# Performance work log

Measured on AMD Instinct MI355X. Metric: run time of the kernel, lower is better.

The kernel has to match this reference:

```python
import jax, jax.numpy as jnp
import numpy as np

LEAKAGE = 0.9
RADIUS = 0.1
AVG_DEGREE = 6


def setup_inputs() -> dict:
    key = jax.random.key(0)
    k1, k2, k3, k4, k5 = jax.random.split(key, 5)
    B, T, I, N, O = 16, 2048, 32, 2048, 32
    input_sequence = jax.random.normal(k1, (B, T, I), dtype=jnp.float32)
    # sparse reservoir matrix, uniform(-1,1) with density avg_degree/N, scaled to spectral radius
    A = jax.random.uniform(k2, (N, N), minval=-1.0, maxval=1.0, dtype=jnp.float32)
    mask = jax.random.uniform(k3, (N, N)) < (AVG_DEGREE / N)
    A = jnp.where(mask, A, 0.0)
    # approximate spectral normalization (power-iteration-free surrogate scale)
    A = A * (RADIUS / jnp.max(jnp.abs(jnp.linalg.eigvals(A))).astype(jnp.float32))
    Win = (RADIUS) * (2.0 * jax.random.uniform(k4, (N, I), dtype=jnp.float32) - 1.0)
    Wout_w = jax.random.normal(k5, (O, N), dtype=jnp.float32) / np.sqrt(N)
    return {"input_sequence": input_sequence, "Win": Win, "A": A, "Wout_w": Wout_w, "washout_len": 64}


def reference(input_sequence, Win, A, Wout_w, washout_len):
    # input projection for all timesteps at once (noise_std = 0.0)
    inp = jnp.einsum('bti,ni->btn', input_sequence, Win)  # [B, T, N]
    B = input_sequence.shape[0]
    N = A.shape[0]
    h0 = jnp.zeros((B, N), dtype=input_sequence.dtype)
    At = A.T

    def step(h, u_t):
        # h: [B, N], u_t: [B, N]
        h_new = (1.0 - LEAKAGE) * h + LEAKAGE * jnp.tanh(h @ At + u_t)
        return h_new, h_new

    _, hs = jax.lax.scan(step, h0, jnp.swapaxes(inp, 0, 1))  # hs: [T, B, N]
    hs = jnp.swapaxes(hs, 0, 1)  # [B, T, N]
    h_list = hs[:, washout_len - 1:]  # keep steps i >= washout_len - 1
    return jnp.einsum('btn,on->bto', h_list, Wout_w)
```

## Files before the change

kernel.cpp:

```cpp
#include <hip/hip_runtime.h>
#include <stdint.h>

#define BB 16
#define TT 2048
#define NI 32
#define NN 2048
#define NO 32
#define WASH 64
#define TO (TT - WASH + 1)
#define W 24
#define WT 24
#define CH 16
#define HBST 2056
#define HBROW 4112
#define UROWB 4136
#define U2OFF 65792
#define LDS_BYTES (U2OFF + CH*UROWB)

typedef short bfvec __attribute__((ext_vector_type(8)));
typedef float f4_t  __attribute__((ext_vector_type(4)));

__device__ inline unsigned short f2bf(float f) {
  unsigned int u = __builtin_bit_cast(unsigned int, f);
  unsigned int r = u + 0x7fffu + ((u >> 16) & 1u);
  return (unsigned short)(r >> 16);
}
__device__ inline float bf2f(unsigned short s) {
  unsigned int u = ((unsigned int)s) << 16;
  return __builtin_bit_cast(float, u);
}
__device__ inline float tanh_fast(float x) {
  x = fminf(15.f, fmaxf(-15.f, x));
  float e = __expf(x + x);
  float r = __builtin_amdgcn_rcpf(e + 1.0f);
  return (e - 1.0f) * r;
}

__global__ void build_ell(const float* __restrict__ A, uint32_t* __restrict__ ell,
                          uint32_t* __restrict__ deg) {
  int gw = (int)((blockIdx.x * blockDim.x + threadIdx.x) >> 6);
  int lane = (int)(threadIdx.x & 63);
  if (gw >= NN) return;
  const float* row = A + (size_t)gw * NN;
  int base = 0;
  for (int c = 0; c < NN; c += 64) {
    float v = row[c + lane];
    bool nz = (v != 0.0f);
    unsigned long long mask = __ballot(nz);
    int pre = __popcll(mask & ((1ull << lane) - 1ull));
    if (nz) {
      int idx = base + pre;
      if (idx < W) {
        uint32_t packed = (((uint32_t)f2bf(v)) << 16) | (uint32_t)((c + lane) * 4);
        ell[(size_t)gw * W + idx] = packed;
      }
    }
    base += __popcll(mask);
  }
  int d = base < W ? base : W;
  if (lane == 0) deg[gw] = (uint32_t)d;
  for (int k = d + lane; k < W; k += 64) ell[(size_t)gw * W + k] = 0u;
}

__global__ void sortperm(const uint32_t* __restrict__ deg, uint32_t* __restrict__ perm,
                         uint32_t* __restrict__ invp) {
  __shared__ int dg[NN];
  int tid = (int)threadIdx.x;
  dg[tid] = (int)deg[tid];
  dg[tid + 1024] = (int)deg[tid + 1024];
  __syncthreads();
  for (int r = tid; r < NN; r += 1024) {
    int d = dg[r];
    int rank = 0;
    for (int j = 0; j < NN; ++j) {
      int dj = dg[j];
      rank += (dj < d) || (dj == d && j < r);
    }
    perm[rank] = (uint32_t)r;
    invp[r] = (uint32_t)rank;
  }
}

__global__ void pairsort(const uint32_t* __restrict__ deg, const uint32_t* __restrict__ perm,
                         uint32_t* __restrict__ pairrank, uint32_t* __restrict__ pp) {
  __shared__ int ps[1024];
  int p = (int)threadIdx.x;
  int d0 = (int)deg[perm[p]]; if (d0 > W) d0 = W;
  int d1 = (int)deg[perm[2047 - p]]; if (d1 > W) d1 = W;
  int s = d0 + d1; if (s > WT) s = WT;
  ps[p] = s;
  __syncthreads();
  int rank = 0;
  for (int j = 0; j < 1024; ++j) {
    int sj = ps[j];
    rank += (sj < s) || (sj == s && j < p);
  }
  pairrank[p] = (uint32_t)rank;
  pp[rank] = (uint32_t)p;
}

__device__ inline int rank2pos(int r, const uint32_t* pairrank) {
  return (r < 1024) ? (2 * (int)pairrank[r]) : (2 * (int)pairrank[2047 - r] + 1);
}

__global__ void build_pairs(const uint32_t* __restrict__ ell, const uint32_t* __restrict__ deg,
                            const uint32_t* __restrict__ perm, const uint32_t* __restrict__ invp,
                            const uint32_t* __restrict__ pairrank, const uint32_t* __restrict__ pp,
                            uint32_t* __restrict__ pa, uint32_t* __restrict__ pva,
                            uint32_t* __restrict__ pvb, uint32_t* __restrict__ wavecnt) {
  int blk = (int)blockIdx.x;
  int lane = (int)threadIdx.x;
  int t = blk * 64 + lane;
  int p = (int)pp[t];
  uint32_t a_[WT], va_[WT], vb_[WT];
  int n = 0;
  int ro = (int)perm[p];
  int d = (int)deg[ro]; if (d > W) d = W;
  for (int k = 0; k < d && n < WT; ++k) {
    uint32_t e = ell[(size_t)ro * W + k];
    int pos = rank2pos((int)invp[(e & 0xffffu) >> 2], pairrank);
    a_[n] = (uint32_t)(pos * 2);
    va_[n] = e & 0xffff0000u;
    vb_[n] = 0u;
    ++n;
  }
  ro = (int)perm[2047 - p];
  d = (int)deg[ro]; if (d > W) d = W;
  for (int k = 0; k < d && n < WT; ++k) {
    uint32_t e = ell[(size_t)ro * W + k];
    int pos = rank2pos((int)invp[(e & 0xffffu) >> 2], pairrank);
    a_[n] = (uint32_t)(pos * 2);
    va_[n] = 0u;
    vb_[n] = e & 0xffff0000u;
    ++n;
  }
  int cnt = n;
  for (; n < WT; ++n) { a_[n] = (uint32_t)(((t + n) & 31) << 2); va_[n] = 0u; vb_[n] = 0u; }
  int m = cnt;
  #pragma unroll
  for (int off = 32; off; off >>= 1) m = max(m, __shfl_xor(m, off));
  if (lane == 0) wavecnt[blk] = (uint32_t)m;
  for (int k = 0; k < WT; ++k) {
    pa[(size_t)t * WT + k] = a_[k];
    pva[(size_t)t * WT + k] = va_[k];
    pvb[(size_t)t * WT + k] = vb_[k];
  }
}

__global__ void build_frags(const float* __restrict__ Win, const float* __restrict__ Wout,
                            const uint32_t* __restrict__ perm, const uint32_t* __restrict__ pp,
                            uint32_t* __restrict__ winf, uint32_t* __restrict__ woutf) {
  int f = (int)(blockIdx.x * blockDim.x + threadIdx.x);
  if (f < 32768) {
    int reg = f & 3, lane = (f >> 2) & 63, ntg = f >> 8;
    int n = (ntg << 4) + (lane & 15);
    int k = ((lane >> 4) << 3) + reg * 2;
    int p = (int)pp[n >> 1];
    int np = (int)perm[(n & 1) ? (2047 - p) : p];
    uint32_t lo = f2bf(Win[(size_t)np * NI + k]);
    uint32_t hi = f2bf(Win[(size_t)np * NI + k + 1]);
    winf[f] = lo | (hi << 16);
  } else {
    int g = f - 32768;
    int reg = g & 3, lane = (g >> 2) & 63, kt = (g >> 8) & 63, ot = g >> 14;
    int o = (ot << 4) + (lane & 15);
    int n = (kt << 5) + ((lane >> 4) << 3) + reg * 2;
    int p = (int)pp[n >> 1];
    int n0 = (int)perm[p];
    int n1 = (int)perm[2047 - p];
    uint32_t lo = f2bf(Wout[(size_t)o * NN + n0]);
    uint32_t hi = f2bf(Wout[(size_t)o * NN + n1]);
    woutf[g] = lo | (hi << 16);
  }
}

#define ENT(K, BASE)                                                                 \
  {                                                                                  \
    float hv = bf2f(*(const unsigned short*)(smem + (BASE) + ea##K));                \
    y0 = __builtin_fmaf(__builtin_bit_cast(float, va##K), hv, y0);                   \
    y1 = __builtin_fmaf(__builtin_bit_cast(float, vb##K), hv, y1);                   \
  }

#define ENTS16(BASE)                                                                 \
  ENT(0, BASE) ENT(1, BASE) ENT(2, BASE) ENT(3, BASE) ENT(4, BASE) ENT(5, BASE)      \
  ENT(6, BASE) ENT(7, BASE) ENT(8, BASE) ENT(9, BASE) ENT(10, BASE) ENT(11, BASE)    \
  ENT(12, BASE) ENT(13, BASE) ENT(14, BASE) ENT(15, BASE)

#define ENTS24(BASE)                                                                 \
  ENTS16(BASE)                                                                       \
  ENT(16, BASE) ENT(17, BASE) ENT(18, BASE) ENT(19, BASE) ENT(20, BASE) ENT(21, BASE)\
  ENT(22, BASE) ENT(23, BASE)

#define STEPBODY(TT, ENTS)                                                           \
  {                                                                                  \
    uint32_t uw = *(const uint32_t*)(smem + u2a + (TT) * UROWB);                     \
    float y0 = bf2f((unsigned short)(uw & 0xffffu));                                 \
    float y1 = bf2f((unsigned short)(uw >> 16));                                     \
    ENTS((((TT) + CH - 1) % CH) * HBROW)                                             \
    float hn0 = 0.1f * h0 + 0.9f * tanh_fast(y0);                                    \
    float hn1 = 0.1f * h1 + 0.9f * tanh_fast(y1);                                    \
    *(uint32_t*)(smem + hwa + (TT) * HBROW) =                                        \
        (uint32_t)f2bf(hn0) | ((uint32_t)f2bf(hn1) << 16);                           \
    h0 = hn0; h1 = hn1;                                                              \
    __syncthreads();                                                                 \
  }

#define S16(TT) STEPBODY(TT, ENTS16)
#define S24(TT) STEPBODY(TT, ENTS24)

__global__ __launch_bounds__(1024, 1) void rec_kernel(
    const float* __restrict__ x,
    const uint32_t* __restrict__ pa, const uint32_t* __restrict__ pva,
    const uint32_t* __restrict__ pvb, const uint32_t* __restrict__ wavecnt,
    const uint32_t* __restrict__ winf, const uint32_t* __restrict__ woutf,
    float* __restrict__ out) {
  extern __shared__ char smem[];
  unsigned short* hb = (unsigned short*)smem;
  float* oscratch = (float*)(smem + U2OFF);

  const int tid = (int)threadIdx.x;
  const int b = (int)blockIdx.x;
  const int lane = tid & 63;
  const int wv = tid >> 6;
  const int la15 = lane & 15;
  const int lg = lane >> 4;
  const int u2a = U2OFF + (tid << 2);
  const int hwa = tid << 2;

  const int cnt = __builtin_amdgcn_readfirstlane((int)wavecnt[wv]);

  uint32_t ea0, ea1, ea2, ea3, ea4, ea5, ea6, ea7, ea8, ea9, ea10, ea11,
           ea12, ea13, ea14, ea15, ea16, ea17, ea18, ea19, ea20, ea21, ea22, ea23;
  uint32_t va0, va1, va2, va3, va4, va5, va6, va7, va8, va9, va10, va11,
           va12, va13, va14, va15, va16, va17, va18, va19, va20, va21, va22, va23;
  uint32_t vb0, vb1, vb2, vb3, vb4, vb5, vb6, vb7, vb8, vb9, vb10, vb11,
           vb12, vb13, vb14, vb15, vb16, vb17, vb18, vb19, vb20, vb21, vb22, vb23;
  {
    const uint4* qa = (const uint4*)(pa + (size_t)tid * WT);
    const uint4* qv = (const uint4*)(pva + (size_t)tid * WT);
    const uint4* qw = (const uint4*)(pvb + (size_t)tid * WT);
    uint4 A0 = qa[0], A1 = qa[1], A2 = qa[2], A3 = qa[3], A4 = qa[4], A5 = qa[5];
    uint4 V0 = qv[0], V1 = qv[1], V2 = qv[2], V3 = qv[3], V4 = qv[4], V5 = qv[5];
    uint4 B0 = qw[0], B1 = qw[1], B2 = qw[2], B3 = qw[3], B4 = qw[4], B5 = qw[5];
    ea0 = A0.x; ea1 = A0.y; ea2 = A0.z; ea3 = A0.w;
    ea4 = A1.x; ea5 = A1.y; ea6 = A1.z; ea7 = A1.w;
    ea8 = A2.x; ea9 = A2.y; ea10 = A2.z; ea11 = A2.w;
    ea12 = A3.x; ea13 = A3.y; ea14 = A3.z; ea15 = A3.w;
    ea16 = A4.x; ea17 = A4.y; ea18 = A4.z; ea19 = A4.w;
    ea20 = A5.x; ea21 = A5.y; ea22 = A5.z; ea23 = A5.w;
    va0 = V0.x; va1 = V0.y; va2 = V0.z; va3 = V0.w;
    va4 = V1.x; va5 = V1.y; va6 = V1.z; va7 = V1.w;
    va8 = V2.x; va9 = V2.y; va10 = V2.z; va11 = V2.w;
    va12 = V3.x; va13 = V3.y; va14 = V3.z; va15 = V3.w;
    va16 = V4.x; va17 = V4.y; va18 = V4.z; va19 = V4.w;
    va20 = V5.x; va21 = V5.y; va22 = V5.z; va23 = V5.w;
    vb0 = B0.x; vb1 = B0.y; vb2 = B0.z; vb3 = B0.w;
    vb4 = B1.x; vb5 = B1.y; vb6 = B1.z; vb7 = B1.w;
    vb8 = B2.x; vb9 = B2.y; vb10 = B2.z; vb11 = B2.w;
    vb12 = B3.x; vb13 = B3.y; vb14 = B3.z; vb15 = B3.w;
    vb16 = B4.x; vb17 = B4.y; vb18 = B4.z; vb19 = B4.w;
    vb20 = B5.x; vb21 = B5.y; vb22 = B5.z; vb23 = B5.w;
  }

  *(uint32_t*)(smem + (CH - 1) * HBROW + (tid << 2)) = 0u;
  float h0 = 0.0f, h1 = 0.0f;

  for (int c = 0; c < TT / CH; ++c) {
    const int t0 = c * CH;

    {
      const float* xp = x + ((size_t)b * TT + (t0 + la15)) * NI + (lg << 3);
      float4 x0 = *(const float4*)xp;
      float4 x1 = *(const float4*)(xp + 4);
      union { unsigned short u16[8]; bfvec v; } af;
      af.u16[0]=f2bf(x0.x); af.u16[1]=f2bf(x0.y); af.u16[2]=f2bf(x0.z); af.u16[3]=f2bf(x0.w);
      af.u16[4]=f2bf(x1.x); af.u16[5]=f2bf(x1.y); af.u16[6]=f2bf(x1.z); af.u16[7]=f2bf(x1.w);
      #pragma unroll
      for (int nt = 0; nt < 8; ++nt) {
        int ntg = (wv << 3) + nt;
        union { uint4 q; bfvec v; } bw;
        bw.q = *(const uint4*)(winf + (((size_t)ntg * 64 + lane) << 2));
        f4_t acc = {0.f, 0.f, 0.f, 0.f};
        acc = __builtin_amdgcn_mfma_f32_16x16x32_bf16(af.v, bw.v, acc, 0, 0, 0);
        int nn = (ntg << 4) + la15;
        int wb = U2OFF + ((nn >> 1) << 2) + ((nn & 1) << 1) + (lg << 2) * UROWB;
        *(unsigned short*)(smem + wb + 0 * UROWB) = f2bf(acc[0]);
        *(unsigned short*)(smem + wb + 1 * UROWB) = f2bf(acc[1]);
        *(unsigned short*)(smem + wb + 2 * UROWB) = f2bf(acc[2]);
        *(unsigned short*)(smem + wb + 3 * UROWB) = f2bf(acc[3]);
      }
    }
    __syncthreads();

    if (cnt <= 16) {
      S16(0)  S16(1)  S16(2)  S16(3)  S16(4)  S16(5)  S16(6)  S16(7)
      S16(8)  S16(9)  S16(10) S16(11) S16(12) S16(13) S16(14) S16(15)
    } else {
      S24(0)  S24(1)  S24(2)  S24(3)  S24(4)  S24(5)  S24(6)  S24(7)
      S24(8)  S24(9)  S24(10) S24(11) S24(12) S24(13) S24(14) S24(15)
    }

    {
      f4_t oa0 = {0.f,0.f,0.f,0.f}, oa1 = {0.f,0.f,0.f,0.f};
      #pragma unroll
      for (int k4 = 0; k4 < 4; ++k4) {
        int kt = (wv << 2) + k4;
        union { uint4 q; bfvec v; } ha, w0, w1;
        ha.q = *(const uint4*)(hb + (size_t)la15 * HBST + (kt << 5) + (lg << 3));
        w0.q = *(const uint4*)(woutf + (((size_t)(kt) * 64 + lane) << 2));
        w1.q = *(const uint4*)(woutf + (((size_t)(64 + kt) * 64 + lane) << 2));
        oa0 = __builtin_amdgcn_mfma_f32_16x16x32_bf16(ha.v, w0.v, oa0, 0, 0, 0);
        oa1 = __builtin_amdgcn_mfma_f32_16x16x32_bf16(ha.v, w1.v, oa1, 0, 0, 0);
      }
      float* os = oscratch + (wv << 9);
      int tb = lg << 2;
      #pragma unroll
      for (int r = 0; r < 4; ++r) os[(tb + r) * 32 + la15] = oa0[r];
      #pragma unroll
      for (int r = 0; r < 4; ++r) os[(tb + r) * 32 + 16 + la15] = oa1[r];
    }
    __syncthreads();
    if (tid < 512) {
      float s = 0.0f;
      #pragma unroll
      for (int w2 = 0; w2 < 16; ++w2) s += oscratch[(w2 << 9) + tid];
      int tg = t0 + (tid >> 5);
      if (tg >= WASH - 1)
        out[((size_t)b * TO + (tg - (WASH - 1))) * NO + (tid & 31)] = s;
    }
    __syncthreads();
  }
}

extern "C" void kernel_launch(void* const* d_in, const int* in_sizes, int n_in,
                              void* d_out, int out_size, void* d_ws, size_t ws_size,
                              hipStream_t stream) {
  (void)in_sizes; (void)n_in; (void)out_size; (void)ws_size;
  const float* x    = (const float*)d_in[0];
  const float* Win  = (const float*)d_in[1];
  const float* A    = (const float*)d_in[2];
  const float* Wout = (const float*)d_in[3];
  float* out = (float*)d_out;

  char* ws = (char*)d_ws;
  uint32_t* ell      = (uint32_t*)(ws);
  uint32_t* deg      = (uint32_t*)(ws + 196608);
  uint32_t* perm     = (uint32_t*)(ws + 204800);
  uint32_t* invp     = (uint32_t*)(ws + 212992);
  uint32_t* pairrank = (uint32_t*)(ws + 221184);
  uint32_t* pp       = (uint32_t*)(ws + 225280);
  uint32_t* wavecnt  = (uint32_t*)(ws + 229376);
  uint32_t* pa       = (uint32_t*)(ws + 229504);
  uint32_t* pva      = (uint32_t*)(ws + 327808);
  uint32_t* pvb      = (uint32_t*)(ws + 426112);
  uint32_t* winf     = (uint32_t*)(ws + 524416);
  uint32_t* woutf    = (uint32_t*)(ws + 655488);

  hipFuncSetAttribute((const void*)rec_kernel,
                      hipFuncAttributeMaxDynamicSharedMemorySize, 160 * 1024);

  hipLaunchKernelGGL(build_ell, dim3(512), dim3(256), 0, stream, A, ell, deg);
  hipLaunchKernelGGL(sortperm, dim3(1), dim3(1024), 0, stream, deg, perm, invp);
  hipLaunchKernelGGL(pairsort, dim3(1), dim3(1024), 0, stream, deg, perm, pairrank, pp);
  hipLaunchKernelGGL(build_pairs, dim3(16), dim3(64), 0, stream,
                     ell, deg, perm, invp, pairrank, pp, pa, pva, pvb, wavecnt);
  hipLaunchKernelGGL(build_frags, dim3(256), dim3(256), 0, stream, Win, Wout, perm, pp, winf, woutf);
  hipLaunchKernelGGL(rec_kernel, dim3(16), dim3(1024), LDS_BYTES, stream,
                     x, pa, pva, pvb, wavecnt, winf, woutf, out);
}
```

Baseline: 3.117 ms.

## Sort gather entries by bank, add finer count-specialized step loops, repack u writes

The pair-building kernel now sorts each thread's gather entries by a lane-rotated LDS bank key, so the 64 lanes of a wave hit distinct banks at each position, and pads with bank-rotated dummy addresses. The recurrent step dispatch adds branches in steps of two entries (8 to 24) instead of only 16 or 24, and each step loop runs un-unrolled to save instruction footprint. The input-projection MFMA swaps its operands so each lane writes packed 32-bit words into the u buffer instead of scattered 16-bit stores, and the u row stride changes to 4132 bytes. The aim is to cut LDS bank conflicts and wasted FMAs per step, at the cost of loop overhead and more code paths.

```diff
diff --git a/kernel.cpp b/kernel.cpp
--- a/kernel.cpp
+++ b/kernel.cpp
@@ -13,7 +13,7 @@
 #define CH 16
 #define HBST 2056
 #define HBROW 4112
-#define UROWB 4136
+#define UROWB 4132
 #define U2OFF 65792
 #define LDS_BYTES (U2OFF + CH*UROWB)
 
@@ -112,7 +112,7 @@
   int lane = (int)threadIdx.x;
   int t = blk * 64 + lane;
   int p = (int)pp[t];
-  uint32_t a_[WT], va_[WT], vb_[WT];
+  uint32_t a_[WT], u_[WT], w_[WT];
   int n = 0;
   int ro = (int)perm[p];
   int d = (int)deg[ro]; if (d > W) d = W;
@@ -120,8 +120,8 @@
     uint32_t e = ell[(size_t)ro * W + k];
     int pos = rank2pos((int)invp[(e & 0xffffu) >> 2], pairrank);
     a_[n] = (uint32_t)(pos * 2);
-    va_[n] = e & 0xffff0000u;
-    vb_[n] = 0u;
+    u_[n] = e & 0xffff0000u;
+    w_[n] = 0u;
     ++n;
   }
   ro = (int)perm[2047 - p];
@@ -130,20 +130,32 @@
     uint32_t e = ell[(size_t)ro * W + k];
     int pos = rank2pos((int)invp[(e & 0xffffu) >> 2], pairrank);
     a_[n] = (uint32_t)(pos * 2);
-    va_[n] = 0u;
-    vb_[n] = e & 0xffff0000u;
+    u_[n] = 0u;
+    w_[n] = e & 0xffff0000u;
     ++n;
   }
   int cnt = n;
-  for (; n < WT; ++n) { a_[n] = (uint32_t)(((t + n) & 31) << 2); va_[n] = 0u; vb_[n] = 0u; }
+  for (int i = 1; i < cnt; ++i) {
+    uint32_t aa = a_[i], uu = u_[i], ww = w_[i];
+    uint32_t key = (((aa >> 2) & 31u) - (uint32_t)lane) & 31u;
+    int j = i - 1;
+    while (j >= 0 && ((((a_[j] >> 2) & 31u) - (uint32_t)lane) & 31u) > key) {
+      a_[j + 1] = a_[j]; u_[j + 1] = u_[j]; w_[j + 1] = w_[j]; --j;
+    }
+    a_[j + 1] = aa; u_[j + 1] = uu; w_[j + 1] = ww;
+  }
+  for (n = cnt; n < WT; ++n) {
+    a_[n] = (uint32_t)(((lane + n) & 31) << 2);
+    u_[n] = 0u; w_[n] = 0u;
+  }
   int m = cnt;
   #pragma unroll
   for (int off = 32; off; off >>= 1) m = max(m, __shfl_xor(m, off));
   if (lane == 0) wavecnt[blk] = (uint32_t)m;
   for (int k = 0; k < WT; ++k) {
     pa[(size_t)t * WT + k] = a_[k];
-    pva[(size_t)t * WT + k] = va_[k];
-    pvb[(size_t)t * WT + k] = vb_[k];
+    pva[(size_t)t * WT + k] = u_[k];
+    pvb[(size_t)t * WT + k] = w_[k];
   }
 }
 
@@ -181,32 +193,31 @@
     y1 = __builtin_fmaf(__builtin_bit_cast(float, vb##K), hv, y1);                   \
   }
 
-#define ENTS16(BASE)                                                                 \
-  ENT(0, BASE) ENT(1, BASE) ENT(2, BASE) ENT(3, BASE) ENT(4, BASE) ENT(5, BASE)      \
-  ENT(6, BASE) ENT(7, BASE) ENT(8, BASE) ENT(9, BASE) ENT(10, BASE) ENT(11, BASE)    \
-  ENT(12, BASE) ENT(13, BASE) ENT(14, BASE) ENT(15, BASE)
-
-#define ENTS24(BASE)                                                                 \
-  ENTS16(BASE)                                                                       \
-  ENT(16, BASE) ENT(17, BASE) ENT(18, BASE) ENT(19, BASE) ENT(20, BASE) ENT(21, BASE)\
-  ENT(22, BASE) ENT(23, BASE)
-
-#define STEPBODY(TT, ENTS)                                                           \
-  {                                                                                  \
-    uint32_t uw = *(const uint32_t*)(smem + u2a + (TT) * UROWB);                     \
+#define ENTS8(B)  ENT(0,B) ENT(1,B) ENT(2,B) ENT(3,B) ENT(4,B) ENT(5,B) ENT(6,B) ENT(7,B)
+#define ENTS10(B) ENTS8(B)  ENT(8,B)  ENT(9,B)
+#define ENTS12(B) ENTS10(B) ENT(10,B) ENT(11,B)
+#define ENTS14(B) ENTS12(B) ENT(12,B) ENT(13,B)
+#define ENTS16(B) ENTS14(B) ENT(14,B) ENT(15,B)
+#define ENTS18(B) ENTS16(B) ENT(16,B) ENT(17,B)
+#define ENTS20(B) ENTS18(B) ENT(18,B) ENT(19,B)
+#define ENTS22(B) ENTS20(B) ENT(20,B) ENT(21,B)
+#define ENTS24(B) ENTS22(B) ENT(22,B) ENT(23,B)
+
+#define STEPLOOP(ENTS)                                                               \
+  _Pragma("unroll 1")                                                                \
+  for (int tt = 0; tt < CH; ++tt) {                                                  \
+    const int po = ((tt + CH - 1) & (CH - 1)) * HBROW;                               \
+    uint32_t uw = *(const uint32_t*)(smem + u2a + tt * UROWB);                       \
     float y0 = bf2f((unsigned short)(uw & 0xffffu));                                 \
     float y1 = bf2f((unsigned short)(uw >> 16));                                     \
-    ENTS((((TT) + CH - 1) % CH) * HBROW)                                             \
+    ENTS(po)                                                                         \
     float hn0 = 0.1f * h0 + 0.9f * tanh_fast(y0);                                    \
     float hn1 = 0.1f * h1 + 0.9f * tanh_fast(y1);                                    \
-    *(uint32_t*)(smem + hwa + (TT) * HBROW) =                                        \
+    *(uint32_t*)(smem + hwa + tt * HBROW) =                                          \
         (uint32_t)f2bf(hn0) | ((uint32_t)f2bf(hn1) << 16);                           \
     h0 = hn0; h1 = hn1;                                                              \
     __syncthreads();                                                                 \
   }
-
-#define S16(TT) STEPBODY(TT, ENTS16)
-#define S24(TT) STEPBODY(TT, ENTS24)
 
 __global__ __launch_bounds__(1024, 1) void rec_kernel(
     const float* __restrict__ x,
@@ -227,7 +238,7 @@
   const int u2a = U2OFF + (tid << 2);
   const int hwa = tid << 2;
 
-  const int cnt = __builtin_amdgcn_readfirstlane((int)wavecnt[wv]);
+  int cnt = __builtin_amdgcn_readfirstlane((int)wavecnt[wv]);
 
   uint32_t ea0, ea1, ea2, ea3, ea4, ea5, ea6, ea7, ea8, ea9, ea10, ea11,
            ea12, ea13, ea14, ea15, ea16, ea17, ea18, ea19, ea20, ea21, ea22, ea23;
@@ -281,24 +292,27 @@
         union { uint4 q; bfvec v; } bw;
         bw.q = *(const uint4*)(winf + (((size_t)ntg * 64 + lane) << 2));
         f4_t acc = {0.f, 0.f, 0.f, 0.f};
-        acc = __builtin_amdgcn_mfma_f32_16x16x32_bf16(af.v, bw.v, acc, 0, 0, 0);
-        int nn = (ntg << 4) + la15;
-        int wb = U2OFF + ((nn >> 1) << 2) + ((nn & 1) << 1) + (lg << 2) * UROWB;
-        *(unsigned short*)(smem + wb + 0 * UROWB) = f2bf(acc[0]);
-        *(unsigned short*)(smem + wb + 1 * UROWB) = f2bf(acc[1]);
-        *(unsigned short*)(smem + wb + 2 * UROWB) = f2bf(acc[2]);
-        *(unsigned short*)(smem + wb + 3 * UROWB) = f2bf(acc[3]);
+        acc = __builtin_amdgcn_mfma_f32_16x16x32_bf16(bw.v, af.v, acc, 0, 0, 0);
+        int dw = (ntg << 3) + (lg << 1);
+        uint32_t w0 = (uint32_t)f2bf(acc[0]) | ((uint32_t)f2bf(acc[1]) << 16);
+        uint32_t w1 = (uint32_t)f2bf(acc[2]) | ((uint32_t)f2bf(acc[3]) << 16);
+        char* ub = smem + U2OFF + la15 * UROWB + (dw << 2);
+        *(uint32_t*)(ub) = w0;
+        *(uint32_t*)(ub + 4) = w1;
       }
     }
     __syncthreads();
 
-    if (cnt <= 16) {
-      S16(0)  S16(1)  S16(2)  S16(3)  S16(4)  S16(5)  S16(6)  S16(7)
-      S16(8)  S16(9)  S16(10) S16(11) S16(12) S16(13) S16(14) S16(15)
-    } else {
-      S24(0)  S24(1)  S24(2)  S24(3)  S24(4)  S24(5)  S24(6)  S24(7)
-      S24(8)  S24(9)  S24(10) S24(11) S24(12) S24(13) S24(14) S24(15)
-    }
+    asm volatile("" : "+s"(cnt));
+    if      (cnt <= 8)  { STEPLOOP(ENTS8)  }
+    else if (cnt <= 10) { STEPLOOP(ENTS10) }
+    else if (cnt <= 12) { STEPLOOP(ENTS12) }
+    else if (cnt <= 14) { STEPLOOP(ENTS14) }
+    else if (cnt <= 16) { STEPLOOP(ENTS16) }
+    else if (cnt <= 18) { STEPLOOP(ENTS18) }
+    else if (cnt <= 20) { STEPLOOP(ENTS20) }
+    else if (cnt <= 22) { STEPLOOP(ENTS22) }
+    else                { STEPLOOP(ENTS24) }
 
     {
       f4_t oa0 = {0.f,0.f,0.f,0.f}, oa1 = {0.f,0.f,0.f,0.f};
```

After: 2.919 ms. 6.3% less time.
